# Performance work log

Measured on AMD Instinct MI355X. Metric: run time of the kernel, lower is better.

Reference implementation:

```python
import jax, jax.numpy as jnp
import numpy as np

B, L, H, E = 32, 512, 8, 64  # L == S == win_size, D == E

def setup_inputs() -> dict:
    key = jax.random.key(0)
    kq, kk, kv, ks = jax.random.split(key, 4)
    return {
        "queries": jax.random.normal(kq, (B, L, H, E), dtype=jnp.float32),
        "keys":    jax.random.normal(kk, (B, L, H, E), dtype=jnp.float32),
        "values":  jax.random.normal(kv, (B, L, H, E), dtype=jnp.float32),
        "sigma":   jax.random.normal(ks, (B, L, H), dtype=jnp.float32),
    }

def reference(queries, keys, values, sigma):
    b, l, h, e = queries.shape
    scale = 1.0 / np.sqrt(e).astype(np.float32)
    # scores: [B,H,L,S]
    attn = scale * jnp.einsum('blhe,bshe->bhls', queries, keys)
    # learned sigma -> Gaussian prior
    sig = jnp.transpose(sigma, (0, 2, 1))            # [B,H,L]
    sig = jax.nn.sigmoid(sig * 5.0) + 1e-5
    sig = jnp.power(3.0, sig) - 1.0
    sig = sig[..., None]                             # [B,H,L,1], broadcast over S (no repeat)
    idx = jnp.arange(l, dtype=jnp.float32)
    dist = jnp.abs(idx[:, None] - idx[None, :])      # [L,S] |i-j| distances buffer
    inv_sqrt_2pi = 1.0 / np.sqrt(2.0 * np.pi).astype(np.float32)
    prior = (inv_sqrt_2pi / sig) * jnp.exp(-(dist ** 2) / (2.0 * sig ** 2))  # [B,H,L,S]
    series = jax.nn.softmax(attn, axis=-1)           # dropout p=0.0 -> identity
    V = jnp.einsum('bhls,bshd->blhd', series, values)
    return V, series, prior
```

## Files before the change

### kernel.cpp

```cpp
#include <hip/hip_runtime.h>
#include <math.h>

#define Bc 32
#define Lc 512
#define Hc 8
#define Ec 64
#define Sc 512

typedef __attribute__((ext_vector_type(8))) short short8;
typedef __attribute__((ext_vector_type(4))) float f32x4;

__device__ inline unsigned short f2bf(float x) {
    unsigned u = __float_as_uint(x);
    return (unsigned short)((u + 0x7fffu + ((u >> 16) & 1u)) >> 16);
}
__device__ inline float bf2f(unsigned short s) {
    return __uint_as_float(((unsigned)s) << 16);
}

__global__ __launch_bounds__(256) void pack_k(const float* __restrict__ src,
                                              unsigned short* __restrict__ hi,
                                              unsigned short* __restrict__ lo) {
    const int t = threadIdx.x;
    const int b = blockIdx.z, h = blockIdx.y, s0 = blockIdx.x * 32;
    const int e4 = (t & 15) * 4;
    const int sr = t >> 4;
    #pragma unroll
    for (int i = 0; i < 2; ++i) {
        const int s = s0 + sr + 16 * i;
        const float4 v = *(const float4*)&src[(((size_t)b * Lc + s) * Hc + h) * Ec + e4];
        ushort4 vh, vl;
        vh.x = f2bf(v.x); vl.x = f2bf(v.x - bf2f(vh.x));
        vh.y = f2bf(v.y); vl.y = f2bf(v.y - bf2f(vh.y));
        vh.z = f2bf(v.z); vl.z = f2bf(v.z - bf2f(vh.z));
        vh.w = f2bf(v.w); vl.w = f2bf(v.w - bf2f(vh.w));
        const size_t o = (((size_t)b * Hc + h) * Lc + s) * Ec + e4;
        *(ushort4*)&hi[o] = vh;
        *(ushort4*)&lo[o] = vl;
    }
}

__global__ __launch_bounds__(256) void pack_vt(const float* __restrict__ V,
                                               unsigned short* __restrict__ Vt) {
    __shared__ float LT[64 * 68];
    const int t = threadIdx.x;
    const int b = blockIdx.z, h = blockIdx.y, s0 = blockIdx.x * 64;
    #pragma unroll
    for (int i = 0; i < 16; ++i) {
        const int idx = t + 256 * i;
        const int e = idx & 63, s = idx >> 6;
        LT[e * 68 + s] = V[(((size_t)b * Lc + s0 + s) * Hc + h) * Ec + e];
    }
    __syncthreads();
    #pragma unroll
    for (int i = 0; i < 16; ++i) {
        const int idx = t + 256 * i;
        const int s = idx & 63, e = idx >> 6;
        Vt[((size_t)(b * Hc + h) * Ec + e) * Sc + s0 + s] = f2bf(LT[e * 68 + s]);
    }
}

__global__ __launch_bounds__(256) void prior_kernel(
    const float* __restrict__ sigma, float* __restrict__ prior)
{
    const int wave = threadIdx.x >> 6;
    const int lane = threadIdx.x & 63;
    const int row  = blockIdx.x * 4 + wave;
    const int l    = row & (Lc - 1);
    const int bh   = row >> 9;
    const int b    = bh >> 3;
    const int h    = bh & (Hc - 1);

    float sg = sigma[((size_t)b * Lc + l) * Hc + h];
    sg = 1.0f / (1.0f + __expf(-5.0f * sg)) + 1e-5f;
    sg = expm1f(sg * 1.0986122886681098f);
    const float inv = 0.3989422804014327f / sg;
    const float c2  = -0.5f / (sg * sg);

    const size_t base = (size_t)row * Sc;
    #pragma unroll
    for (int i = 0; i < 2; ++i) {
        const int s0 = i * 256 + lane * 4;
        const float d0 = (float)(l - (s0 + 0));
        const float d1 = (float)(l - (s0 + 1));
        const float d2 = (float)(l - (s0 + 2));
        const float d3 = (float)(l - (s0 + 3));
        float4 o;
        o.x = inv * __expf(c2 * d0 * d0);
        o.y = inv * __expf(c2 * d1 * d1);
        o.z = inv * __expf(c2 * d2 * d2);
        o.w = inv * __expf(c2 * d3 * d3);
        *(float4*)&prior[base + s0] = o;
    }
}

__global__ __launch_bounds__(256, 2) void attn_mfma(
    const float* __restrict__ Q, const unsigned short* __restrict__ Khi,
    const unsigned short* __restrict__ Klo, const unsigned short* __restrict__ Vt,
    float* __restrict__ outV, float* __restrict__ series)
{
    const int t    = threadIdx.x;
    const int lane = t & 63, wave = t >> 6;
    const int quad = lane >> 4, l16 = lane & 15;

    const int bid = blockIdx.x;
    const int xcd = bid & 7;
    const int rr  = bid >> 3;
    const int xt  = rr & 7;
    const int bh  = (rr >> 3) * 8 + xcd;
    const int b = bh >> 3, h = bh & 7;
    const int l = xt * 64 + wave * 16 + l16;

    const size_t kb = (size_t)bh * Lc * Ec;

    short8 qh[2], ql[2];
    {
        const float* qp = &Q[(((size_t)b * Lc + l) * Hc + h) * Ec + quad * 8];
        #pragma unroll
        for (int kt = 0; kt < 2; ++kt) {
            const float4 v0 = *(const float4*)(qp + kt * 32);
            const float4 v1 = *(const float4*)(qp + kt * 32 + 4);
            const float vv[8] = {v0.x, v0.y, v0.z, v0.w, v1.x, v1.y, v1.z, v1.w};
            #pragma unroll
            for (int j = 0; j < 8; ++j) {
                const unsigned short hb = f2bf(vv[j]);
                qh[kt][j] = (short)hb;
                ql[kt][j] = (short)f2bf(vv[j] - bf2f(hb));
            }
        }
    }

    f32x4 acc[32];
    #pragma unroll
    for (int nt = 0; nt < 32; ++nt) { acc[nt][0]=0.f; acc[nt][1]=0.f; acc[nt][2]=0.f; acc[nt][3]=0.f; }

    const int arow = (l16 >> 2) * 8 + (l16 & 3);
    #pragma unroll
    for (int nt = 0; nt < 32; ++nt) {
        const int s = (nt >> 1) * 32 + arow + (nt & 1) * 4;
        const unsigned short* kp = &Khi[kb + (size_t)s * Ec + quad * 8];
        const unsigned short* lp = &Klo[kb + (size_t)s * Ec + quad * 8];
        #pragma unroll
        for (int kt = 0; kt < 2; ++kt) {
            const short8 kh = *(const short8*)(kp + kt * 32);
            const short8 kl = *(const short8*)(lp + kt * 32);
            acc[nt] = __builtin_amdgcn_mfma_f32_16x16x32_bf16(kh, qh[kt], acc[nt], 0, 0, 0);
            acc[nt] = __builtin_amdgcn_mfma_f32_16x16x32_bf16(kl, qh[kt], acc[nt], 0, 0, 0);
            acc[nt] = __builtin_amdgcn_mfma_f32_16x16x32_bf16(kh, ql[kt], acc[nt], 0, 0, 0);
        }
    }

    float mx = acc[0][0];
    #pragma unroll
    for (int nt = 0; nt < 32; ++nt) {
        #pragma unroll
        for (int r4 = 0; r4 < 4; ++r4) mx = fmaxf(mx, acc[nt][r4]);
    }
    mx = fmaxf(mx, __shfl_xor(mx, 16));
    mx = fmaxf(mx, __shfl_xor(mx, 32));
    float ssum = 0.f;
    #pragma unroll
    for (int nt = 0; nt < 32; ++nt) {
        #pragma unroll
        for (int r4 = 0; r4 < 4; ++r4) {
            const float e = __expf((acc[nt][r4] - mx) * 0.125f);
            acc[nt][r4] = e; ssum += e;
        }
    }
    ssum += __shfl_xor(ssum, 16);
    ssum += __shfl_xor(ssum, 32);
    const float is = 1.f / ssum;
    #pragma unroll
    for (int nt = 0; nt < 32; ++nt) {
        acc[nt][0] *= is; acc[nt][1] *= is; acc[nt][2] *= is; acc[nt][3] *= is;
    }

    f32x4 oaccT[4];
    #pragma unroll
    for (int et = 0; et < 4; ++et) { oaccT[et][0]=0.f; oaccT[et][1]=0.f; oaccT[et][2]=0.f; oaccT[et][3]=0.f; }

    const unsigned short* vb = &Vt[(size_t)bh * Ec * Sc];
    float* srow = &series[((size_t)bh * Lc + l) * Sc];
    #pragma unroll
    for (int t2 = 0; t2 < 16; ++t2) {
        const f32x4 p0 = acc[2 * t2];
        const f32x4 p1 = acc[2 * t2 + 1];
        *(f32x4*)&srow[t2 * 32 + quad * 8]     = p0;
        *(f32x4*)&srow[t2 * 32 + quad * 8 + 4] = p1;
        short8 pb;
        pb[0] = (short)f2bf(p0[0]); pb[1] = (short)f2bf(p0[1]);
        pb[2] = (short)f2bf(p0[2]); pb[3] = (short)f2bf(p0[3]);
        pb[4] = (short)f2bf(p1[0]); pb[5] = (short)f2bf(p1[1]);
        pb[6] = (short)f2bf(p1[2]); pb[7] = (short)f2bf(p1[3]);
        #pragma unroll
        for (int et = 0; et < 4; ++et) {
            const short8 vf = *(const short8*)&vb[(size_t)(et * 16 + l16) * Sc + t2 * 32 + quad * 8];
            oaccT[et] = __builtin_amdgcn_mfma_f32_16x16x32_bf16(vf, pb, oaccT[et], 0, 0, 0);
        }
    }

    #pragma unroll
    for (int et = 0; et < 4; ++et) {
        float4 o;
        o.x = oaccT[et][0]; o.y = oaccT[et][1]; o.z = oaccT[et][2]; o.w = oaccT[et][3];
        *(float4*)&outV[(((size_t)b * Lc + l) * Hc + h) * Ec + et * 16 + quad * 4] = o;
    }
}

extern "C" void kernel_launch(void* const* d_in, const int* in_sizes, int n_in,
                              void* d_out, int out_size, void* d_ws, size_t ws_size,
                              hipStream_t stream) {
    (void)d_ws; (void)ws_size; (void)n_in; (void)in_sizes; (void)out_size;
    const float* Q  = (const float*)d_in[0];
    const float* K  = (const float*)d_in[1];
    const float* Vv = (const float*)d_in[2];
    const float* sg = (const float*)d_in[3];

    float* outV   = (float*)d_out;
    float* series = outV + (size_t)Bc * Lc * Hc * Ec;
    float* prior  = series + (size_t)Bc * Hc * Lc * Sc;

    unsigned short* Khi = (unsigned short*)prior;
    unsigned short* Klo = Khi + (size_t)Bc * Hc * Lc * Ec;
    unsigned short* Vt  = Klo + (size_t)Bc * Hc * Lc * Ec;

    pack_k <<<dim3(Lc / 32, Hc, Bc), 256, 0, stream>>>(K, Khi, Klo);
    pack_vt<<<dim3(Lc / 64, Hc, Bc), 256, 0, stream>>>(Vv, Vt);
    attn_mfma<<<dim3((Bc * Hc * Lc) / 64 / 4, 1, 1), 256, 0, stream>>>(Q, Khi, Klo, Vt, outV, series);
    prior_kernel<<<(Bc * Hc * Lc) / 4, 256, 0, stream>>>(sg, prior);
}
```

Before: 628.3 us.

## Split key range across wave pairs, fuse prior into attention, use nontemporal stores

The attention kernel now handles 32 query rows per block, with two waves each covering half of the 512 keys. Row max, row sum and the partial PV outputs are combined through shared memory, which halves accumulator registers and raises the occupancy hint to 4. When a large enough workspace is available, the packed K/V scratch moves there so the prior computation can be fused into the attention kernel instead of running as a separate pass. Series, output and prior writes use nontemporal stores to avoid cache pollution; the cost is extra block-level syncs and a fallback path when no workspace is given.

```diff
diff --git a/kernel.cpp b/kernel.cpp
--- a/kernel.cpp
+++ b/kernel.cpp
@@ -85,33 +85,43 @@
         const float d1 = (float)(l - (s0 + 1));
         const float d2 = (float)(l - (s0 + 2));
         const float d3 = (float)(l - (s0 + 3));
-        float4 o;
-        o.x = inv * __expf(c2 * d0 * d0);
-        o.y = inv * __expf(c2 * d1 * d1);
-        o.z = inv * __expf(c2 * d2 * d2);
-        o.w = inv * __expf(c2 * d3 * d3);
-        *(float4*)&prior[base + s0] = o;
-    }
-}
-
-__global__ __launch_bounds__(256, 2) void attn_mfma(
+        f32x4 o;
+        o[0] = inv * __expf(c2 * d0 * d0);
+        o[1] = inv * __expf(c2 * d1 * d1);
+        o[2] = inv * __expf(c2 * d2 * d2);
+        o[3] = inv * __expf(c2 * d3 * d3);
+        __builtin_nontemporal_store(o, (f32x4*)&prior[base + s0]);
+    }
+}
+
+template<int FUSE_PRIOR>
+__global__ __launch_bounds__(256, 4) void attn_mfma(
     const float* __restrict__ Q, const unsigned short* __restrict__ Khi,
     const unsigned short* __restrict__ Klo, const unsigned short* __restrict__ Vt,
-    float* __restrict__ outV, float* __restrict__ series)
+    const float* __restrict__ sigma,
+    float* __restrict__ outV, float* __restrict__ series, float* __restrict__ prior)
 {
+    __shared__ float smx[4][16];
+    __shared__ float ssm[4][16];
+    __shared__ float ex[2][64][16];
+
     const int t    = threadIdx.x;
     const int lane = t & 63, wave = t >> 6;
     const int quad = lane >> 4, l16 = lane & 15;
+    const int hs   = wave & 1;
+    const int rg   = wave >> 1;
 
     const int bid = blockIdx.x;
     const int xcd = bid & 7;
     const int rr  = bid >> 3;
-    const int xt  = rr & 7;
-    const int bh  = (rr >> 3) * 8 + xcd;
+    const int xt  = rr & 15;
+    const int bh  = (rr >> 4) * 8 + xcd;
     const int b = bh >> 3, h = bh & 7;
-    const int l = xt * 64 + wave * 16 + l16;
+    const int l0 = xt * 32;
+    const int l  = l0 + rg * 16 + l16;
 
     const size_t kb = (size_t)bh * Lc * Ec;
+    const int sbase = hs * 256;
 
     short8 qh[2], ql[2];
     {
@@ -130,14 +140,14 @@
         }
     }
 
-    f32x4 acc[32];
-    #pragma unroll
-    for (int nt = 0; nt < 32; ++nt) { acc[nt][0]=0.f; acc[nt][1]=0.f; acc[nt][2]=0.f; acc[nt][3]=0.f; }
+    f32x4 acc[16];
+    #pragma unroll
+    for (int nt = 0; nt < 16; ++nt) { acc[nt][0]=0.f; acc[nt][1]=0.f; acc[nt][2]=0.f; acc[nt][3]=0.f; }
 
     const int arow = (l16 >> 2) * 8 + (l16 & 3);
     #pragma unroll
-    for (int nt = 0; nt < 32; ++nt) {
-        const int s = (nt >> 1) * 32 + arow + (nt & 1) * 4;
+    for (int nt = 0; nt < 16; ++nt) {
+        const int s = sbase + (nt >> 1) * 32 + arow + (nt & 1) * 4;
         const unsigned short* kp = &Khi[kb + (size_t)s * Ec + quad * 8];
         const unsigned short* lp = &Klo[kb + (size_t)s * Ec + quad * 8];
         #pragma unroll
@@ -152,15 +162,19 @@
 
     float mx = acc[0][0];
     #pragma unroll
-    for (int nt = 0; nt < 32; ++nt) {
+    for (int nt = 0; nt < 16; ++nt) {
         #pragma unroll
         for (int r4 = 0; r4 < 4; ++r4) mx = fmaxf(mx, acc[nt][r4]);
     }
     mx = fmaxf(mx, __shfl_xor(mx, 16));
     mx = fmaxf(mx, __shfl_xor(mx, 32));
+    if (lane < 16) smx[wave][lane] = mx;
+    __syncthreads();
+    mx = fmaxf(mx, smx[wave ^ 1][l16]);
+
     float ssum = 0.f;
     #pragma unroll
-    for (int nt = 0; nt < 32; ++nt) {
+    for (int nt = 0; nt < 16; ++nt) {
         #pragma unroll
         for (int r4 = 0; r4 < 4; ++r4) {
             const float e = __expf((acc[nt][r4] - mx) * 0.125f);
@@ -169,9 +183,12 @@
     }
     ssum += __shfl_xor(ssum, 16);
     ssum += __shfl_xor(ssum, 32);
+    if (lane < 16) ssm[wave][lane] = ssum;
+    __syncthreads();
+    ssum += ssm[wave ^ 1][l16];
     const float is = 1.f / ssum;
     #pragma unroll
-    for (int nt = 0; nt < 32; ++nt) {
+    for (int nt = 0; nt < 16; ++nt) {
         acc[nt][0] *= is; acc[nt][1] *= is; acc[nt][2] *= is; acc[nt][3] *= is;
     }
 
@@ -180,13 +197,13 @@
     for (int et = 0; et < 4; ++et) { oaccT[et][0]=0.f; oaccT[et][1]=0.f; oaccT[et][2]=0.f; oaccT[et][3]=0.f; }
 
     const unsigned short* vb = &Vt[(size_t)bh * Ec * Sc];
-    float* srow = &series[((size_t)bh * Lc + l) * Sc];
-    #pragma unroll
-    for (int t2 = 0; t2 < 16; ++t2) {
+    float* srow = &series[((size_t)bh * Lc + l) * Sc + sbase];
+    #pragma unroll
+    for (int t2 = 0; t2 < 8; ++t2) {
         const f32x4 p0 = acc[2 * t2];
         const f32x4 p1 = acc[2 * t2 + 1];
-        *(f32x4*)&srow[t2 * 32 + quad * 8]     = p0;
-        *(f32x4*)&srow[t2 * 32 + quad * 8 + 4] = p1;
+        __builtin_nontemporal_store(p0, (f32x4*)&srow[t2 * 32 + quad * 8]);
+        __builtin_nontemporal_store(p1, (f32x4*)&srow[t2 * 32 + quad * 8 + 4]);
         short8 pb;
         pb[0] = (short)f2bf(p0[0]); pb[1] = (short)f2bf(p0[1]);
         pb[2] = (short)f2bf(p0[2]); pb[3] = (short)f2bf(p0[3]);
@@ -194,23 +211,58 @@
         pb[6] = (short)f2bf(p1[2]); pb[7] = (short)f2bf(p1[3]);
         #pragma unroll
         for (int et = 0; et < 4; ++et) {
-            const short8 vf = *(const short8*)&vb[(size_t)(et * 16 + l16) * Sc + t2 * 32 + quad * 8];
+            const short8 vf = *(const short8*)&vb[(size_t)(et * 16 + l16) * Sc + sbase + t2 * 32 + quad * 8];
             oaccT[et] = __builtin_amdgcn_mfma_f32_16x16x32_bf16(vf, pb, oaccT[et], 0, 0, 0);
         }
     }
 
-    #pragma unroll
-    for (int et = 0; et < 4; ++et) {
-        float4 o;
-        o.x = oaccT[et][0]; o.y = oaccT[et][1]; o.z = oaccT[et][2]; o.w = oaccT[et][3];
-        *(float4*)&outV[(((size_t)b * Lc + l) * Hc + h) * Ec + et * 16 + quad * 4] = o;
+    if (hs == 1) {
+        #pragma unroll
+        for (int et = 0; et < 4; ++et)
+            *(f32x4*)&ex[rg][lane][et * 4] = oaccT[et];
+    }
+    __syncthreads();
+    if (hs == 0) {
+        #pragma unroll
+        for (int et = 0; et < 4; ++et) {
+            const f32x4 p = *(const f32x4*)&ex[rg][lane][et * 4];
+            f32x4 o;
+            o[0] = oaccT[et][0] + p[0]; o[1] = oaccT[et][1] + p[1];
+            o[2] = oaccT[et][2] + p[2]; o[3] = oaccT[et][3] + p[3];
+            __builtin_nontemporal_store(o,
+                (f32x4*)&outV[(((size_t)b * Lc + l) * Hc + h) * Ec + et * 16 + quad * 4]);
+        }
+    }
+
+    if (FUSE_PRIOR) {
+        #pragma unroll
+        for (int r_ = 0; r_ < 8; ++r_) {
+            const int lrow = l0 + wave * 8 + r_;
+            float sg = sigma[((size_t)b * Lc + lrow) * Hc + h];
+            sg = 1.0f / (1.0f + __expf(-5.0f * sg)) + 1e-5f;
+            sg = expm1f(sg * 1.0986122886681098f);
+            const float inv = 0.3989422804014327f / sg;
+            const float c2  = -0.5f / (sg * sg);
+            const int c0 = lane * 8;
+            f32x4 o0, o1;
+            #pragma unroll
+            for (int j = 0; j < 4; ++j) {
+                const float d0 = (float)(lrow - (c0 + j));
+                const float d1 = (float)(lrow - (c0 + 4 + j));
+                o0[j] = inv * __expf(c2 * d0 * d0);
+                o1[j] = inv * __expf(c2 * d1 * d1);
+            }
+            float* pp = &prior[((size_t)bh * Lc + lrow) * Sc + c0];
+            __builtin_nontemporal_store(o0, (f32x4*)pp);
+            __builtin_nontemporal_store(o1, (f32x4*)(pp + 4));
+        }
     }
 }
 
 extern "C" void kernel_launch(void* const* d_in, const int* in_sizes, int n_in,
                               void* d_out, int out_size, void* d_ws, size_t ws_size,
                               hipStream_t stream) {
-    (void)d_ws; (void)ws_size; (void)n_in; (void)in_sizes; (void)out_size;
+    (void)n_in; (void)in_sizes; (void)out_size;
     const float* Q  = (const float*)d_in[0];
     const float* K  = (const float*)d_in[1];
     const float* Vv = (const float*)d_in[2];
@@ -220,12 +272,27 @@
     float* series = outV + (size_t)Bc * Lc * Hc * Ec;
     float* prior  = series + (size_t)Bc * Hc * Lc * Sc;
 
-    unsigned short* Khi = (unsigned short*)prior;
-    unsigned short* Klo = Khi + (size_t)Bc * Hc * Lc * Ec;
-    unsigned short* Vt  = Klo + (size_t)Bc * Hc * Lc * Ec;
+    const size_t plane = (size_t)Bc * Hc * Lc * Ec;
+    const size_t scratch_bytes = plane * 2 * 3;
+
+    unsigned short *Khi, *Klo, *Vt;
+    const bool use_ws = (d_ws != nullptr) && (ws_size >= scratch_bytes);
+    if (use_ws) {
+        Khi = (unsigned short*)d_ws;
+    } else {
+        Khi = (unsigned short*)prior;
+    }
+    Klo = Khi + plane;
+    Vt  = Klo + plane;
 
     pack_k <<<dim3(Lc / 32, Hc, Bc), 256, 0, stream>>>(K, Khi, Klo);
     pack_vt<<<dim3(Lc / 64, Hc, Bc), 256, 0, stream>>>(Vv, Vt);
-    attn_mfma<<<dim3((Bc * Hc * Lc) / 64 / 4, 1, 1), 256, 0, stream>>>(Q, Khi, Klo, Vt, outV, series);
-    prior_kernel<<<(Bc * Hc * Lc) / 4, 256, 0, stream>>>(sg, prior);
-}
+    if (use_ws) {
+        attn_mfma<1><<<dim3((Bc * Hc * Lc) / 32, 1, 1), 256, 0, stream>>>(
+            Q, Khi, Klo, Vt, sg, outV, series, prior);
+    } else {
+        attn_mfma<0><<<dim3((Bc * Hc * Lc) / 32, 1, 1), 256, 0, stream>>>(
+            Q, Khi, Klo, Vt, sg, outV, series, prior);
+        prior_kernel<<<(Bc * Hc * Lc) / 4, 256, 0, stream>>>(sg, prior);
+    }
+}
```

After: 793.8 us. 1.26x slower.
